# Kernel tuning notes

Measured on AMD Instinct MI355X. Metric: run time of the kernel, lower is better.

Reference implementation:

```python
import jax, jax.numpy as jnp
import numpy as np
import math

B_SZ, T_LEN, DIM = 1, 1024, 1024
D_STATE, EXPAND, NUM_SCALES, CONV_K = 16, 2, 3, 4
D_INNER = EXPAND * DIM
EPS_LOG = 1e-38
LN_EPS = 1e-5


def _causal_dwconv(x, w, b):
    # x: (B,T,D), w: (D,1,K) depthwise, b: (D,). torch Conv1d(pad=K-1)[:, :, :T] == left-pad K-1 (causal).
    y = jax.lax.conv_general_dilated(
        jnp.transpose(x, (0, 2, 1)), w, window_strides=(1,),
        padding=[(CONV_K - 1, 0)], dimension_numbers=('NCH', 'OIH', 'NCH'),
        feature_group_count=w.shape[0])
    return jnp.transpose(y, (0, 2, 1)) + b


def _ssm_core(x, cw, cb, xw, dtw, dtb, Dp):
    # x: (B,T,d_inner)
    xc = jax.nn.silu(_causal_dwconv(x, cw, cb))
    proj = xc @ xw.T                               # (B,T,2*d_state)
    B_ssm, C_ssm = proj[..., :D_STATE], proj[..., D_STATE:]
    dt = jax.nn.softplus(B_ssm @ dtw.T + dtb)      # (B,T,d_inner)
    dt = jax.nn.softplus(dt)                       # selective_scan applies softplus a second time (faithful)
    A = -jnp.arange(1, D_STATE + 1, dtype=xc.dtype)  # (d_state,) == -A_init row, same for every d_inner channel
    dA = jnp.exp(dt[..., None] * A)                # (B,T,d_inner,d_state)
    dBx = dt[..., None] * B_ssm[:, :, None, :] * xc[..., None]
    log_dA = jnp.log(jnp.clip(dA, EPS_LOG))
    log_dBx = jnp.log(jnp.clip(dBx, EPS_LOG))
    # parallel_scan_cpu: h = exp(cumsum(log_dA) + logcumsumexp(log_dBx - cumsum(log_dA)))
    a_star = jnp.cumsum(log_dA, axis=1)
    h = jnp.exp(a_star + jax.lax.cumlogsumexp(log_dBx - a_star, axis=1))
    return jnp.einsum('bts,btds->btd', C_ssm, h) + Dp * xc


def _downsample(x, stride):
    if stride == 1:
        return x
    Bb, T, D = x.shape
    Tt = (T // stride) * stride
    return x[:, :Tt].reshape(Bb, Tt // stride, stride, D).mean(2)


def _upsample(x, T_out):
    # F.interpolate(mode='linear', align_corners=False)
    T_in = x.shape[1]
    if T_in == T_out:
        return x
    scale = T_in / T_out
    pos = jnp.clip((jnp.arange(T_out, dtype=jnp.float32) + 0.5) * scale - 0.5, 0.0, T_in - 1)
    lo = jnp.floor(pos).astype(jnp.int32)
    hi = jnp.minimum(lo + 1, T_in - 1)
    w = (pos - lo.astype(pos.dtype))[None, :, None]
    return x[:, lo] * (1.0 - w) + x[:, hi] * w


def _forward(x, in_proj_w, conv_w, conv_b, xproj_w, dtproj_w, dtproj_b,
             D_param, scale_weights, gate_w1, gate_w2, out_proj_w, ln_g, ln_b):
    residual = x
    xz = x @ in_proj_w.T                           # (B,T,2*d_inner)
    x_in, gate = xz[..., :D_INNER], xz[..., D_INNER:]
    outs = []
    for s in range(NUM_SCALES):
        x_s = _downsample(x_in, 2 ** s)
        y_s = _ssm_core(x_s, conv_w[s], conv_b[s], xproj_w[s], dtproj_w[s], dtproj_b[s], D_param[s])
        outs.append(_upsample(y_s, x.shape[1]))
    w = jax.nn.softmax(scale_weights)
    fused = sum(w[s] * outs[s] for s in range(NUM_SCALES))
    ctx = sum(outs) / NUM_SCALES
    gate_ctx = jax.nn.sigmoid(jax.nn.silu(ctx @ gate_w1.T) @ gate_w2.T)
    out = (fused * gate_ctx) * jax.nn.silu(gate)
    out = out @ out_proj_w.T
    y = out + residual
    mu = y.mean(-1, keepdims=True)
    var = ((y - mu) ** 2).mean(-1, keepdims=True)
    return (y - mu) / jnp.sqrt(var + LN_EPS) * ln_g + ln_b


def setup_inputs() -> dict:
    key = jax.random.key(0)
    ks = jax.random.split(key, 12)
    g = lambda k, shp, s: (jax.random.normal(k, shp, jnp.float32) * s)
    return {
        'x': g(ks[0], (B_SZ, T_LEN, DIM), 1.0),
        'in_proj_w': g(ks[1], (2 * D_INNER, DIM), DIM ** -0.5),
        'conv_w': g(ks[2], (NUM_SCALES, D_INNER, 1, CONV_K), CONV_K ** -0.5),
        'conv_b': g(ks[3], (NUM_SCALES, D_INNER), 0.02),
        'xproj_w': g(ks[4], (NUM_SCALES, 2 * D_STATE, D_INNER), D_INNER ** -0.5),
        'dtproj_w': g(ks[5], (NUM_SCALES, D_INNER, D_STATE), D_STATE ** -0.5),
        'dtproj_b': jax.random.uniform(ks[6], (NUM_SCALES, D_INNER), jnp.float32,
                                       math.log(0.001), math.log(0.1)),
        'D_param': jnp.ones((NUM_SCALES, D_INNER), jnp.float32),
        'scale_weights': jnp.ones((NUM_SCALES,), jnp.float32) / NUM_SCALES,
        'gate_w1': g(ks[7], (D_INNER // 2, D_INNER), D_INNER ** -0.5),
        'gate_w2': g(ks[8], (D_INNER, D_INNER // 2), (D_INNER // 2) ** -0.5),
        'out_proj_w': g(ks[9], (DIM, D_INNER), D_INNER ** -0.5),
        'ln_g': jnp.ones((DIM,), jnp.float32),
        'ln_b': jnp.zeros((DIM,), jnp.float32),
    }


def reference(x, in_proj_w, conv_w, conv_b, xproj_w, dtproj_w, dtproj_b,
              D_param, scale_weights, gate_w1, gate_w2, out_proj_w, ln_g, ln_b):
    return _forward(x, in_proj_w, conv_w, conv_b, xproj_w, dtproj_w, dtproj_b,
                    D_param, scale_weights, gate_w1, gate_w2, out_proj_w, ln_g, ln_b)
```

## Files before the change

kernel.cpp:

```cpp
#include <hip/hip_runtime.h>

typedef unsigned short u16;
typedef float floatx4 __attribute__((ext_vector_type(4)));
typedef short shortx8 __attribute__((ext_vector_type(8)));

#define DIN 2048

__device__ __forceinline__ u16 f2bf(float f){
  unsigned u = __float_as_uint(f);
  u = (u + 0x7fffu + ((u>>16)&1u))>>16;
  return (u16)u;
}
__device__ __forceinline__ float sigf(float x){ return 1.f/(1.f+__expf(-x)); }
__device__ __forceinline__ float siluf(float x){ return x*sigf(x); }
__device__ __forceinline__ float softplusf(float x){ return fmaxf(x,0.f)+log1pf(__expf(-fabsf(x))); }

__device__ __forceinline__ void gld_lds16(const void* g, void* l){
  __builtin_amdgcn_global_load_lds((const __attribute__((address_space(1))) unsigned*)g,
                                   (__attribute__((address_space(3))) unsigned*)l, 16, 0, 0);
}

#define OFF_WINP  0ull
#define OFF_WG1   8388608ull
#define OFF_WG2   12582912ull
#define OFF_WOP   16777216ull
#define OFF_XB    20971520ull
#define OFF_XIN   23068672ull
#define OFF_SGATE 31457280ull
#define OFF_X1    39845888ull
#define OFF_X2    44040192ull
#define OFF_XC0   46137344ull
#define OFF_XC1   54525952ull
#define OFF_XC2   58720256ull
#define OFF_DT0   60817408ull
#define OFF_DT1   69206016ull
#define OFF_DT2   73400320ull
#define OFF_Y0    75497472ull
#define OFF_Y1    83886080ull
#define OFF_Y2    88080384ull
#define OFF_P0    90177536ull
#define OFF_P1    90308608ull
#define OFF_P2    90374144ull
#define OFF_CTXB  OFF_XC0
#define OFF_T1B   OFF_XC1
#define OFF_FUSED OFF_DT0
#define OFF_G3O   OFF_DT1
#define OFF_YPRE  OFF_Y0
#define OFF_PS    OFF_Y0
#define OFF_HINIT OFF_XIN

__global__ __launch_bounds__(256) void cvt_kernel(
    const float* __restrict__ s0, u16* __restrict__ d0,
    const float* __restrict__ s1, u16* __restrict__ d1,
    const float* __restrict__ s2, u16* __restrict__ d2,
    const float* __restrict__ s3, u16* __restrict__ d3,
    const float* __restrict__ s4, u16* __restrict__ d4)
{
  int i = (blockIdx.x*256 + threadIdx.x)*4;
  const float* s; u16* d;
  if      (i <  4194304){ s=s0; d=d0; }
  else if (i <  6291456){ s=s1; d=d1; i -=  4194304; }
  else if (i <  8388608){ s=s2; d=d2; i -=  6291456; }
  else if (i < 10485760){ s=s3; d=d3; i -=  8388608; }
  else                  { s=s4; d=d4; i -= 10485760; }
  const float4 v = *(const float4*)(s + i);
  ushort4 o; o.x = f2bf(v.x); o.y = f2bf(v.y); o.z = f2bf(v.z); o.w = f2bf(v.w);
  *(ushort4*)(d + i) = o;
}

template<int MODE, int BM>
__global__ __launch_bounds__(256) void gemm_bt(
    const u16* __restrict__ A, const u16* __restrict__ B,
    int M, int N, int K,
    float* __restrict__ out_f, float* __restrict__ out_f2, u16* __restrict__ out_b,
    float* __restrict__ ex0, float* __restrict__ ex1)
{
  constexpr int NI = BM/32;
  constexpr int IP = BM/64;
  __shared__ u16 smA[2][BM*32];
  __shared__ u16 smB[2][BM*32];
  const int tid  = threadIdx.x;
  const int m0   = blockIdx.y * BM;
  const int n0   = blockIdx.x * BM;
  const int wv   = tid >> 6;
  const int lane = tid & 63;
  const int mw   = (wv >> 1) * (BM/2);
  const int nw   = (wv & 1) * (BM/2);
  const int quad = lane >> 4;
  const int l16  = lane & 15;
  const int srow = tid >> 2;
  const int scol = (tid & 3) * 8;

  floatx4 acc[NI][NI];
#pragma unroll
  for (int i=0;i<NI;i++)
#pragma unroll
    for (int j=0;j<NI;j++) acc[i][j] = (floatx4)0.f;

  auto stage = [&](int buf, int k0){
#pragma unroll
    for (int p=0;p<IP;p++){
      gld_lds16(A + (size_t)(m0 + p*64 + srow)*K + k0 + scol, &smA[buf][p*2048 + wv*512]);
      gld_lds16(B + (size_t)(n0 + p*64 + srow)*K + k0 + scol, &smB[buf][p*2048 + wv*512]);
    }
  };

  stage(0, 0);
  int cur = 0;
  for (int k0 = 0; k0 < K; k0 += 32) {
    __syncthreads();
    if (k0 + 32 < K) stage(cur^1, k0+32);
    shortx8 af[NI], bfr[NI];
#pragma unroll
    for (int i=0;i<NI;i++){
      af[i]  = *(const shortx8*)&smA[cur][(mw + i*16 + l16)*32 + quad*8];
      bfr[i] = *(const shortx8*)&smB[cur][(nw + i*16 + l16)*32 + quad*8];
    }
#pragma unroll
    for (int i=0;i<NI;i++)
#pragma unroll
      for (int j=0;j<NI;j++)
        acc[i][j] = __builtin_amdgcn_mfma_f32_16x16x32_bf16(af[i], bfr[j], acc[i][j], 0, 0, 0);
    cur ^= 1;
  }

#pragma unroll
  for (int i=0;i<NI;i++){
    const int mb = m0 + mw + i*16 + quad*4;
#pragma unroll
    for (int j=0;j<NI;j++){
      const int n = n0 + nw + j*16 + l16;
      const floatx4 v4 = acc[i][j];
      if (MODE == 0){
        if (n < 2048){
#pragma unroll
          for (int r=0;r<4;r++) out_f[(size_t)(mb+r)*2048 + n] = v4[r];
          ex0[(size_t)(mb>>1)*2048 + n]       = 0.5f*(v4[0]+v4[1]);
          ex0[(size_t)((mb>>1)+1)*2048 + n]   = 0.5f*(v4[2]+v4[3]);
          ex1[(size_t)(mb>>2)*2048 + n]       = 0.25f*(v4[0]+v4[1]+v4[2]+v4[3]);
        } else {
#pragma unroll
          for (int r=0;r<4;r++) out_f2[(size_t)(mb+r)*2048 + (n-2048)] = siluf(v4[r]);
        }
      } else if (MODE == 1){
#pragma unroll
        for (int r=0;r<4;r++) out_b[(size_t)(mb+r)*N + n] = f2bf(siluf(v4[r]));
      } else if (MODE == 2){
#pragma unroll
        for (int r=0;r<4;r++){
          const size_t idx = (size_t)(mb+r)*N + n;
          out_b[idx] = f2bf(sigf(v4[r]) * ex0[idx] * ex1[idx]);
        }
      } else {
#pragma unroll
        for (int r=0;r<4;r++){
          const size_t idx = (size_t)(mb+r)*N + n;
          out_f[idx] = v4[r] + ex0[idx];
        }
      }
    }
  }
}

__global__ __launch_bounds__(256) void conv_kernel(const float* __restrict__ xin,
    const float* __restrict__ x1, const float* __restrict__ x2,
    const float* __restrict__ cw, const float* __restrict__ cb,
    float* __restrict__ xc0, float* __restrict__ xc1, float* __restrict__ xc2){
  const int idx = blockIdx.x*256 + threadIdx.x;
  const float* xs; float* xc; int s, local;
  if (idx < 1024*DIN)              { s=0; local=idx;             xs=xin; xc=xc0; }
  else if (idx < (1024+512)*DIN)   { s=1; local=idx-1024*DIN;    xs=x1;  xc=xc1; }
  else                             { s=2; local=idx-1536*DIN;    xs=x2;  xc=xc2; }
  const int t = local >> 11, d = local & 2047;
  const float* w = cw + ((size_t)(s*DIN) + d)*4;
  float acc = cb[s*DIN + d];
#pragma unroll
  for (int j=0;j<4;j++){
    const int tt = t - 3 + j;
    if (tt >= 0) acc += w[j] * xs[(size_t)tt*DIN + d];
  }
  xc[local] = siluf(acc);
}

__global__ __launch_bounds__(256) void xproj_kernel(const float* __restrict__ xc0,
    const float* __restrict__ xc1, const float* __restrict__ xc2,
    const float* __restrict__ xw,
    float* __restrict__ p0, float* __restrict__ p1, float* __restrict__ p2){
  __shared__ float srow[DIN];
  const int b = blockIdx.x;
  const float* xc; float* proj; int s, t;
  if (b < 1024)      { s=0; t=b;       xc=xc0; proj=p0; }
  else if (b < 1536) { s=1; t=b-1024;  xc=xc1; proj=p1; }
  else               { s=2; t=b-1536;  xc=xc2; proj=p2; }
  const float* xr = xc + (size_t)t*DIN;
  const int tid = threadIdx.x;
#pragma unroll
  for (int q=0;q<2;q++){
    const int k = (q*256 + tid)*4;
    *(float4*)&srow[k] = *(const float4*)&xr[k];
  }
  __syncthreads();
  const int i = tid >> 3;
  const int j = tid & 7;
  const float* w = xw + ((size_t)s*32 + i)*DIN;
  float acc = 0.f;
#pragma unroll 8
  for (int c=0;c<256;c++){
    const int k = j + 8*c;
    acc += srow[k]*w[k];
  }
  acc += __shfl_xor(acc,1); acc += __shfl_xor(acc,2); acc += __shfl_xor(acc,4);
  if (j == 0) proj[t*32 + i] = acc;
}

__global__ __launch_bounds__(256) void dtproj_kernel(const float* __restrict__ p0,
    const float* __restrict__ p1, const float* __restrict__ p2,
    const float* __restrict__ dtw, const float* __restrict__ dtb,
    float* __restrict__ dt0, float* __restrict__ dt1, float* __restrict__ dt2){
  const int idx = blockIdx.x*256 + threadIdx.x;
  const float* proj; float* dt; int s, local;
  if (idx < 1024*DIN)            { s=0; local=idx;          proj=p0; dt=dt0; }
  else if (idx < (1024+512)*DIN) { s=1; local=idx-1024*DIN; proj=p1; dt=dt1; }
  else                           { s=2; local=idx-1536*DIN; proj=p2; dt=dt2; }
  const int t = local >> 11, d = local & 2047;
  const float* w  = dtw + ((size_t)(s*DIN) + d)*16;
  const float* pr = proj + t*32;
  float acc = dtb[s*DIN + d];
#pragma unroll
  for (int n=0;n<16;n++) acc += pr[n]*w[n];
  dt[local] = softplusf(softplusf(acc));
}

__global__ __launch_bounds__(256) void scan_p1(
    const float* __restrict__ xc0, const float* __restrict__ xc1, const float* __restrict__ xc2,
    const float* __restrict__ p0,  const float* __restrict__ p1,  const float* __restrict__ p2,
    const float* __restrict__ dt0, const float* __restrict__ dt1, const float* __restrict__ dt2,
    float2* __restrict__ PS)
{
  __shared__ float sproj[32*32];
  int b = blockIdx.x;
  const float *xc, *proj, *dt; int base;
  if (b < 256)      { xc=xc0; proj=p0; dt=dt0; base=0; }
  else if (b < 384) { b-=256; xc=xc1; proj=p1; dt=dt1; base=32; }
  else              { b-=384; xc=xc2; proj=p2; dt=dt2; base=48; }
  const int chunk = b >> 3;
  const int d     = (b & 7)*256 + threadIdx.x;
  const int t0    = chunk*32;
  {
    const int k = threadIdx.x*4;
    *(float4*)&sproj[k] = *(const float4*)&proj[t0*32 + k];
  }
  __syncthreads();

  float H[16], P[16];
#pragma unroll
  for (int n=0;n<16;n++){ H[n]=0.f; P[n]=1.f; }
  const float* dtp = dt + (size_t)t0*DIN + d;
  const float* xcp = xc + (size_t)t0*DIN + d;
  float dtn = dtp[0], xcn = xcp[0];
  for (int tt=0; tt<32; tt++){
    const float dtv = dtn, xcv = xcn;
    if (tt < 31){ dtn = dtp[(size_t)(tt+1)*DIN]; xcn = xcp[(size_t)(tt+1)*DIN]; }
    const float e = __expf(-dtv);
    const float c = dtv*xcv;
    const float* Bp = &sproj[tt*32];
    float ep = e;
#pragma unroll
    for (int n=0;n<16;n++){
      const float dA  = fmaxf(ep, 1e-38f);
      const float dBx = fmaxf(c*Bp[n], 1e-38f);
      H[n] = dA*H[n] + dBx;
      P[n] *= dA;
      ep *= e;
    }
  }
  float2* o = PS + ((size_t)(base+chunk)*2048 + d)*16;
#pragma unroll
  for (int n=0;n<16;n++){ float2 v; v.x=P[n]; v.y=H[n]; o[n]=v; }
}

__global__ __launch_bounds__(256) void scan_combine(const float2* __restrict__ PS,
                                                    float* __restrict__ Hinit){
  int id = blockIdx.x*256 + threadIdx.x;
  int base, C;
  if (id < 32768)      { base=0;  C=32; }
  else if (id < 65536) { id-=32768; base=32; C=16; }
  else                 { id-=65536; base=48; C=8;  }
  const size_t off = (size_t)base*32768 + id;
  const float2* ps = PS + off;
  float* hi = Hinit + off;
  float H = 0.f;
  for (int c=0;c<C;c++){
    hi[(size_t)c*32768] = H;
    const float2 v = ps[(size_t)c*32768];
    H = v.x*H + v.y;
  }
}

__global__ __launch_bounds__(256) void scan_p2(
    const float* __restrict__ xc0, const float* __restrict__ xc1, const float* __restrict__ xc2,
    const float* __restrict__ p0,  const float* __restrict__ p1,  const float* __restrict__ p2,
    const float* __restrict__ dt0, const float* __restrict__ dt1, const float* __restrict__ dt2,
    const float* __restrict__ Hinit, const float* __restrict__ Dp_all,
    float* __restrict__ y0, float* __restrict__ y1, float* __restrict__ y2)
{
  __shared__ float sproj[32*32];
  int b = blockIdx.x;
  const float *xc, *proj, *dt; float* y; int base, s;
  if (b < 256)      { xc=xc0; proj=p0; dt=dt0; y=y0; base=0;  s=0; }
  else if (b < 384) { b-=256; xc=xc1; proj=p1; dt=dt1; y=y1; base=32; s=1; }
  else              { b-=384; xc=xc2; proj=p2; dt=dt2; y=y2; base=48; s=2; }
  const int chunk = b >> 3;
  const int d     = (b & 7)*256 + threadIdx.x;
  const int t0    = chunk*32;
  {
    const int k = threadIdx.x*4;
    *(float4*)&sproj[k] = *(const float4*)&proj[t0*32 + k];
  }
  __syncthreads();

  float H[16];
  const float* hi = Hinit + ((size_t)(base+chunk)*2048 + d)*16;
#pragma unroll
  for (int n=0;n<16;n++) H[n] = hi[n];
  const float Dv = Dp_all[s*DIN + d];
  const float* dtp = dt + (size_t)t0*DIN + d;
  const float* xcp = xc + (size_t)t0*DIN + d;
  float* yp = y + (size_t)t0*DIN + d;
  float dtn = dtp[0], xcn = xcp[0];
  for (int tt=0; tt<32; tt++){
    const float dtv = dtn, xcv = xcn;
    if (tt < 31){ dtn = dtp[(size_t)(tt+1)*DIN]; xcn = xcp[(size_t)(tt+1)*DIN]; }
    const float e = __expf(-dtv);
    const float c = dtv*xcv;
    const float* Bp = &sproj[tt*32];
    float ep = e;
    float pacc = 0.f;
#pragma unroll
    for (int n=0;n<16;n++){
      const float dA  = fmaxf(ep, 1e-38f);
      const float dBx = fmaxf(c*Bp[n], 1e-38f);
      H[n] = dA*H[n] + dBx;
      pacc += Bp[16+n]*H[n];
      ep *= e;
    }
    yp[(size_t)tt*DIN] = pacc + Dv*xcv;
  }
}

__device__ __forceinline__ float ups_read(const float* __restrict__ ys, int Tin, int t, int d){
  const float scale = (float)Tin * (1.f/1024.f);
  float pos = ((float)t + 0.5f)*scale - 0.5f;
  pos = fminf(fmaxf(pos, 0.f), (float)(Tin-1));
  const int lo = (int)floorf(pos);
  const float w = pos - (float)lo;
  const int hi = min(lo+1, Tin-1);
  return ys[(size_t)lo*DIN + d]*(1.f-w) + ys[(size_t)hi*DIN + d]*w;
}

__global__ __launch_bounds__(256) void fuse_kernel(const float* __restrict__ y0,
    const float* __restrict__ y1, const float* __restrict__ y2,
    const float* __restrict__ sw, u16* __restrict__ ctxb, float* __restrict__ fused){
  const int idx = blockIdx.x*256 + threadIdx.x;
  const int t = idx >> 11, d = idx & 2047;
  const float w0r = sw[0], w1r = sw[1], w2r = sw[2];
  const float mx = fmaxf(w0r, fmaxf(w1r, w2r));
  float e0 = __expf(w0r-mx), e1 = __expf(w1r-mx), e2 = __expf(w2r-mx);
  const float inv = 1.f/(e0+e1+e2);
  e0 *= inv; e1 *= inv; e2 *= inv;
  const float o0 = y0[idx];
  const float o1 = ups_read(y1, 512, t, d);
  const float o2 = ups_read(y2, 256, t, d);
  fused[idx] = e0*o0 + e1*o1 + e2*o2;
  ctxb[idx]  = f2bf((o0+o1+o2)*(1.f/3.f));
}

__global__ __launch_bounds__(256) void ln_kernel(const float* __restrict__ ypre,
    const float* __restrict__ g, const float* __restrict__ b, float* __restrict__ out){
  __shared__ float red[4];
  const int t = blockIdx.x;
  const float* row = ypre + (size_t)t*1024;
  float v[4];
  float s = 0.f;
#pragma unroll
  for (int i=0;i<4;i++){ v[i] = row[threadIdx.x + i*256]; s += v[i]; }
  s += __shfl_xor(s,1); s += __shfl_xor(s,2); s += __shfl_xor(s,4);
  s += __shfl_xor(s,8); s += __shfl_xor(s,16); s += __shfl_xor(s,32);
  if ((threadIdx.x & 63) == 0) red[threadIdx.x>>6] = s;
  __syncthreads();
  const float mu = (red[0]+red[1]+red[2]+red[3]) * (1.f/1024.f);
  __syncthreads();
  float q = 0.f;
#pragma unroll
  for (int i=0;i<4;i++){ const float dd = v[i]-mu; q += dd*dd; }
  q += __shfl_xor(q,1); q += __shfl_xor(q,2); q += __shfl_xor(q,4);
  q += __shfl_xor(q,8); q += __shfl_xor(q,16); q += __shfl_xor(q,32);
  if ((threadIdx.x & 63) == 0) red[threadIdx.x>>6] = q;
  __syncthreads();
  const float rstd = rsqrtf((red[0]+red[1]+red[2]+red[3]) * (1.f/1024.f) + 1e-5f);
#pragma unroll
  for (int i=0;i<4;i++){
    const int c = threadIdx.x + i*256;
    out[(size_t)t*1024 + c] = (v[i]-mu)*rstd*g[c] + b[c];
  }
}

extern "C" void kernel_launch(void* const* d_in, const int* in_sizes, int n_in,
                              void* d_out, int out_size, void* d_ws, size_t ws_size,
                              hipStream_t stream) {
  const float* x     = (const float*)d_in[0];
  const float* inpw  = (const float*)d_in[1];
  const float* convw = (const float*)d_in[2];
  const float* convb = (const float*)d_in[3];
  const float* xpw   = (const float*)d_in[4];
  const float* dtw   = (const float*)d_in[5];
  const float* dtb   = (const float*)d_in[6];
  const float* Dp    = (const float*)d_in[7];
  const float* sw    = (const float*)d_in[8];
  const float* gw1   = (const float*)d_in[9];
  const float* gw2   = (const float*)d_in[10];
  const float* opw   = (const float*)d_in[11];
  const float* lng   = (const float*)d_in[12];
  const float* lnb   = (const float*)d_in[13];
  float* out = (float*)d_out;

  char* ws = (char*)d_ws;
  u16*    wInp  = (u16*)   (ws + OFF_WINP);
  u16*    wG1   = (u16*)   (ws + OFF_WG1);
  u16*    wG2   = (u16*)   (ws + OFF_WG2);
  u16*    wOp   = (u16*)   (ws + OFF_WOP);
  u16*    xb    = (u16*)   (ws + OFF_XB);
  float*  xin   = (float*) (ws + OFF_XIN);
  float*  sgate = (float*) (ws + OFF_SGATE);
  float*  x1    = (float*) (ws + OFF_X1);
  float*  x2    = (float*) (ws + OFF_X2);
  float*  xc0   = (float*) (ws + OFF_XC0);
  float*  xc1   = (float*) (ws + OFF_XC1);
  float*  xc2   = (float*) (ws + OFF_XC2);
  float*  dt0   = (float*) (ws + OFF_DT0);
  float*  dt1   = (float*) (ws + OFF_DT1);
  float*  dt2   = (float*) (ws + OFF_DT2);
  float*  y0    = (float*) (ws + OFF_Y0);
  float*  y1    = (float*) (ws + OFF_Y1);
  float*  y2    = (float*) (ws + OFF_Y2);
  float*  p0    = (float*) (ws + OFF_P0);
  float*  p1    = (float*) (ws + OFF_P1);
  float*  p2    = (float*) (ws + OFF_P2);
  float2* PS    = (float2*)(ws + OFF_PS);
  float*  Hinit = (float*) (ws + OFF_HINIT);
  u16*    ctxb  = (u16*)   (ws + OFF_CTXB);
  u16*    t1b   = (u16*)   (ws + OFF_T1B);
  float*  fused = (float*) (ws + OFF_FUSED);
  u16*    g3o   = (u16*)   (ws + OFF_G3O);
  float*  ypre  = (float*) (ws + OFF_YPRE);

  cvt_kernel<<<11264, 256, 0, stream>>>(inpw, wInp, gw1, wG1, gw2, wG2, opw, wOp, x, xb);
  gemm_bt<0,128><<<dim3(32, 8), 256, 0, stream>>>(xb, wInp, 1024, 4096, 1024,
                                                  xin, sgate, nullptr, x1, x2);
  conv_kernel<<<(1792*DIN)/256, 256, 0, stream>>>(xin, x1, x2, convw, convb, xc0, xc1, xc2);
  xproj_kernel<<<1792, 256, 0, stream>>>(xc0, xc1, xc2, xpw, p0, p1, p2);
  dtproj_kernel<<<(1792*DIN)/256, 256, 0, stream>>>(p0, p1, p2, dtw, dtb, dt0, dt1, dt2);
  scan_p1<<<448, 256, 0, stream>>>(xc0, xc1, xc2, p0, p1, p2, dt0, dt1, dt2, PS);
  scan_combine<<<384, 256, 0, stream>>>(PS, Hinit);
  scan_p2<<<448, 256, 0, stream>>>(xc0, xc1, xc2, p0, p1, p2, dt0, dt1, dt2,
                                   Hinit, Dp, y0, y1, y2);
  fuse_kernel<<<(1024*DIN)/256, 256, 0, stream>>>(y0, y1, y2, sw, ctxb, fused);
  gemm_bt<1,64><<<dim3(16, 16), 256, 0, stream>>>(ctxb, wG1, 1024, 1024, 2048,
                                                  nullptr, nullptr, t1b, nullptr, nullptr);
  gemm_bt<2,64><<<dim3(32, 16), 256, 0, stream>>>(t1b, wG2, 1024, 2048, 1024,
                                                  nullptr, nullptr, g3o, fused, sgate);
  gemm_bt<3,64><<<dim3(16, 16), 256, 0, stream>>>(g3o, wOp, 1024, 1024, 2048,
                                                  ypre, nullptr, nullptr, const_cast<float*>(x), nullptr);
  ln_kernel<<<1024, 256, 0, stream>>>(ypre, lng, lnb, out);
}
```

Measured before the change: 340.9 us.

## Fuse dt projection into scan kernels and split-K the K=2048 GEMMs

Removes the standalone dtproj kernel and its three dt buffers, recomputing dt inside both scan passes from register-held dt weights and the staged projection. This avoids writing and twice re-reading a large fp32 dt tensor at the cost of recomputing the projection in each pass. The gate-1 and output-projection GEMMs use 2-way split-K to put more blocks in flight, adding a small epilogue kernel for gate-1 and folding the partial sums plus residual into the layernorm kernel. The in_proj GEMM switches from 128 to 64 tiles with more blocks.

```diff
diff --git a/kernel.cpp b/kernel.cpp
--- a/kernel.cpp
+++ b/kernel.cpp
@@ -32,9 +32,8 @@
 #define OFF_XC0   46137344ull
 #define OFF_XC1   54525952ull
 #define OFF_XC2   58720256ull
-#define OFF_DT0   60817408ull
-#define OFF_DT1   69206016ull
-#define OFF_DT2   73400320ull
+#define OFF_FUSED 60817408ull
+#define OFF_G3O   69206016ull
 #define OFF_Y0    75497472ull
 #define OFF_Y1    83886080ull
 #define OFF_Y2    88080384ull
@@ -43,11 +42,12 @@
 #define OFF_P2    90374144ull
 #define OFF_CTXB  OFF_XC0
 #define OFF_T1B   OFF_XC1
-#define OFF_FUSED OFF_DT0
-#define OFF_G3O   OFF_DT1
-#define OFF_YPRE  OFF_Y0
 #define OFF_PS    OFF_Y0
 #define OFF_HINIT OFF_XIN
+#define OFF_T1A0  OFF_XIN
+#define OFF_T1A1  OFF_X1
+#define OFF_YPA0  OFF_Y1
+#define OFF_YPA1  (OFF_XC0 + 4194304ull)
 
 __global__ __launch_bounds__(256) void cvt_kernel(
     const float* __restrict__ s0, u16* __restrict__ d0,
@@ -71,8 +71,9 @@
 template<int MODE, int BM>
 __global__ __launch_bounds__(256) void gemm_bt(
     const u16* __restrict__ A, const u16* __restrict__ B,
-    int M, int N, int K,
+    int N, int K, int Ks,
     float* __restrict__ out_f, float* __restrict__ out_f2, u16* __restrict__ out_b,
+    const float* __restrict__ ex0f, const float* __restrict__ ex1f,
     float* __restrict__ ex0, float* __restrict__ ex1)
 {
   constexpr int NI = BM/32;
@@ -97,6 +98,9 @@
 #pragma unroll
     for (int j=0;j<NI;j++) acc[i][j] = (floatx4)0.f;
 
+  const int kStart = blockIdx.z * Ks;
+  const int kEnd   = kStart + Ks;
+
   auto stage = [&](int buf, int k0){
 #pragma unroll
     for (int p=0;p<IP;p++){
@@ -105,11 +109,11 @@
     }
   };
 
-  stage(0, 0);
+  stage(0, kStart);
   int cur = 0;
-  for (int k0 = 0; k0 < K; k0 += 32) {
+  for (int k0 = kStart; k0 < kEnd; k0 += 32) {
     __syncthreads();
-    if (k0 + 32 < K) stage(cur^1, k0+32);
+    if (k0 + 32 < kEnd) stage(cur^1, k0+32);
     shortx8 af[NI], bfr[NI];
 #pragma unroll
     for (int i=0;i<NI;i++){
@@ -142,24 +146,30 @@
 #pragma unroll
           for (int r=0;r<4;r++) out_f2[(size_t)(mb+r)*2048 + (n-2048)] = siluf(v4[r]);
         }
-      } else if (MODE == 1){
-#pragma unroll
-        for (int r=0;r<4;r++) out_b[(size_t)(mb+r)*N + n] = f2bf(siluf(v4[r]));
       } else if (MODE == 2){
 #pragma unroll
         for (int r=0;r<4;r++){
           const size_t idx = (size_t)(mb+r)*N + n;
-          out_b[idx] = f2bf(sigf(v4[r]) * ex0[idx] * ex1[idx]);
+          out_b[idx] = f2bf(sigf(v4[r]) * ex0f[idx] * ex1f[idx]);
         }
       } else {
-#pragma unroll
-        for (int r=0;r<4;r++){
-          const size_t idx = (size_t)(mb+r)*N + n;
-          out_f[idx] = v4[r] + ex0[idx];
-        }
+        float* dst = blockIdx.z ? out_f2 : out_f;
+#pragma unroll
+        for (int r=0;r<4;r++) dst[(size_t)(mb+r)*N + n] = v4[r];
       }
     }
   }
+}
+
+__global__ __launch_bounds__(256) void g2_epi(const float* __restrict__ a,
+    const float* __restrict__ b, u16* __restrict__ o){
+  const int i = (blockIdx.x*256 + threadIdx.x)*4;
+  const float4 va = *(const float4*)(a+i);
+  const float4 vb = *(const float4*)(b+i);
+  ushort4 r;
+  r.x = f2bf(siluf(va.x+vb.x)); r.y = f2bf(siluf(va.y+vb.y));
+  r.z = f2bf(siluf(va.z+vb.z)); r.w = f2bf(siluf(va.w+vb.w));
+  *(ushort4*)(o+i) = r;
 }
 
 __global__ __launch_bounds__(256) void conv_kernel(const float* __restrict__ xin,
@@ -213,36 +223,18 @@
   if (j == 0) proj[t*32 + i] = acc;
 }
 
-__global__ __launch_bounds__(256) void dtproj_kernel(const float* __restrict__ p0,
-    const float* __restrict__ p1, const float* __restrict__ p2,
-    const float* __restrict__ dtw, const float* __restrict__ dtb,
-    float* __restrict__ dt0, float* __restrict__ dt1, float* __restrict__ dt2){
-  const int idx = blockIdx.x*256 + threadIdx.x;
-  const float* proj; float* dt; int s, local;
-  if (idx < 1024*DIN)            { s=0; local=idx;          proj=p0; dt=dt0; }
-  else if (idx < (1024+512)*DIN) { s=1; local=idx-1024*DIN; proj=p1; dt=dt1; }
-  else                           { s=2; local=idx-1536*DIN; proj=p2; dt=dt2; }
-  const int t = local >> 11, d = local & 2047;
-  const float* w  = dtw + ((size_t)(s*DIN) + d)*16;
-  const float* pr = proj + t*32;
-  float acc = dtb[s*DIN + d];
-#pragma unroll
-  for (int n=0;n<16;n++) acc += pr[n]*w[n];
-  dt[local] = softplusf(softplusf(acc));
-}
-
 __global__ __launch_bounds__(256) void scan_p1(
     const float* __restrict__ xc0, const float* __restrict__ xc1, const float* __restrict__ xc2,
     const float* __restrict__ p0,  const float* __restrict__ p1,  const float* __restrict__ p2,
-    const float* __restrict__ dt0, const float* __restrict__ dt1, const float* __restrict__ dt2,
+    const float* __restrict__ dtw, const float* __restrict__ dtb,
     float2* __restrict__ PS)
 {
   __shared__ float sproj[32*32];
   int b = blockIdx.x;
-  const float *xc, *proj, *dt; int base;
-  if (b < 256)      { xc=xc0; proj=p0; dt=dt0; base=0; }
-  else if (b < 384) { b-=256; xc=xc1; proj=p1; dt=dt1; base=32; }
-  else              { b-=384; xc=xc2; proj=p2; dt=dt2; base=48; }
+  const float *xc, *proj; int base, s;
+  if (b < 256)      { xc=xc0; proj=p0; base=0;  s=0; }
+  else if (b < 384) { b-=256; xc=xc1; proj=p1; base=32; s=1; }
+  else              { b-=384; xc=xc2; proj=p2; base=48; s=2; }
   const int chunk = b >> 3;
   const int d     = (b & 7)*256 + threadIdx.x;
   const int t0    = chunk*32;
@@ -252,18 +244,27 @@
   }
   __syncthreads();
 
+  float wreg[16];
+  const float* wr = dtw + ((size_t)(s*DIN) + d)*16;
+#pragma unroll
+  for (int n=0;n<16;n++) wreg[n] = wr[n];
+  const float bias = dtb[s*DIN + d];
+
   float H[16], P[16];
 #pragma unroll
   for (int n=0;n<16;n++){ H[n]=0.f; P[n]=1.f; }
-  const float* dtp = dt + (size_t)t0*DIN + d;
   const float* xcp = xc + (size_t)t0*DIN + d;
-  float dtn = dtp[0], xcn = xcp[0];
+  float xcn = xcp[0];
   for (int tt=0; tt<32; tt++){
-    const float dtv = dtn, xcv = xcn;
-    if (tt < 31){ dtn = dtp[(size_t)(tt+1)*DIN]; xcn = xcp[(size_t)(tt+1)*DIN]; }
+    const float xcv = xcn;
+    if (tt < 31) xcn = xcp[(size_t)(tt+1)*DIN];
+    const float* Bp = &sproj[tt*32];
+    float bs = bias;
+#pragma unroll
+    for (int n=0;n<16;n++) bs += Bp[n]*wreg[n];
+    const float dtv = softplusf(softplusf(bs));
     const float e = __expf(-dtv);
     const float c = dtv*xcv;
-    const float* Bp = &sproj[tt*32];
     float ep = e;
 #pragma unroll
     for (int n=0;n<16;n++){
@@ -300,16 +301,16 @@
 __global__ __launch_bounds__(256) void scan_p2(
     const float* __restrict__ xc0, const float* __restrict__ xc1, const float* __restrict__ xc2,
     const float* __restrict__ p0,  const float* __restrict__ p1,  const float* __restrict__ p2,
-    const float* __restrict__ dt0, const float* __restrict__ dt1, const float* __restrict__ dt2,
+    const float* __restrict__ dtw, const float* __restrict__ dtb,
     const float* __restrict__ Hinit, const float* __restrict__ Dp_all,
     float* __restrict__ y0, float* __restrict__ y1, float* __restrict__ y2)
 {
   __shared__ float sproj[32*32];
   int b = blockIdx.x;
-  const float *xc, *proj, *dt; float* y; int base, s;
-  if (b < 256)      { xc=xc0; proj=p0; dt=dt0; y=y0; base=0;  s=0; }
-  else if (b < 384) { b-=256; xc=xc1; proj=p1; dt=dt1; y=y1; base=32; s=1; }
-  else              { b-=384; xc=xc2; proj=p2; dt=dt2; y=y2; base=48; s=2; }
+  const float *xc, *proj; float* y; int base, s;
+  if (b < 256)      { xc=xc0; proj=p0; y=y0; base=0;  s=0; }
+  else if (b < 384) { b-=256; xc=xc1; proj=p1; y=y1; base=32; s=1; }
+  else              { b-=384; xc=xc2; proj=p2; y=y2; base=48; s=2; }
   const int chunk = b >> 3;
   const int d     = (b & 7)*256 + threadIdx.x;
   const int t0    = chunk*32;
@@ -319,21 +320,30 @@
   }
   __syncthreads();
 
+  float wreg[16];
+  const float* wr = dtw + ((size_t)(s*DIN) + d)*16;
+#pragma unroll
+  for (int n=0;n<16;n++) wreg[n] = wr[n];
+  const float bias = dtb[s*DIN + d];
+
   float H[16];
   const float* hi = Hinit + ((size_t)(base+chunk)*2048 + d)*16;
 #pragma unroll
   for (int n=0;n<16;n++) H[n] = hi[n];
   const float Dv = Dp_all[s*DIN + d];
-  const float* dtp = dt + (size_t)t0*DIN + d;
   const float* xcp = xc + (size_t)t0*DIN + d;
   float* yp = y + (size_t)t0*DIN + d;
-  float dtn = dtp[0], xcn = xcp[0];
+  float xcn = xcp[0];
   for (int tt=0; tt<32; tt++){
-    const float dtv = dtn, xcv = xcn;
-    if (tt < 31){ dtn = dtp[(size_t)(tt+1)*DIN]; xcn = xcp[(size_t)(tt+1)*DIN]; }
+    const float xcv = xcn;
+    if (tt < 31) xcn = xcp[(size_t)(tt+1)*DIN];
+    const float* Bp = &sproj[tt*32];
+    float bs = bias;
+#pragma unroll
+    for (int n=0;n<16;n++) bs += Bp[n]*wreg[n];
+    const float dtv = softplusf(softplusf(bs));
     const float e = __expf(-dtv);
     const float c = dtv*xcv;
-    const float* Bp = &sproj[tt*32];
     float ep = e;
     float pacc = 0.f;
 #pragma unroll
@@ -375,15 +385,20 @@
   ctxb[idx]  = f2bf((o0+o1+o2)*(1.f/3.f));
 }
 
-__global__ __launch_bounds__(256) void ln_kernel(const float* __restrict__ ypre,
+__global__ __launch_bounds__(256) void ln_kernel(const float* __restrict__ ya,
+    const float* __restrict__ yb, const float* __restrict__ xr,
     const float* __restrict__ g, const float* __restrict__ b, float* __restrict__ out){
   __shared__ float red[4];
   const int t = blockIdx.x;
-  const float* row = ypre + (size_t)t*1024;
+  const size_t ro = (size_t)t*1024;
   float v[4];
   float s = 0.f;
 #pragma unroll
-  for (int i=0;i<4;i++){ v[i] = row[threadIdx.x + i*256]; s += v[i]; }
+  for (int i=0;i<4;i++){
+    const int c = threadIdx.x + i*256;
+    v[i] = ya[ro+c] + yb[ro+c] + xr[ro+c];
+    s += v[i];
+  }
   s += __shfl_xor(s,1); s += __shfl_xor(s,2); s += __shfl_xor(s,4);
   s += __shfl_xor(s,8); s += __shfl_xor(s,16); s += __shfl_xor(s,32);
   if ((threadIdx.x & 63) == 0) red[threadIdx.x>>6] = s;
@@ -401,7 +416,7 @@
 #pragma unroll
   for (int i=0;i<4;i++){
     const int c = threadIdx.x + i*256;
-    out[(size_t)t*1024 + c] = (v[i]-mu)*rstd*g[c] + b[c];
+    out[ro + c] = (v[i]-mu)*rstd*g[c] + b[c];
   }
 }
 
@@ -437,9 +452,6 @@
   float*  xc0   = (float*) (ws + OFF_XC0);
   float*  xc1   = (float*) (ws + OFF_XC1);
   float*  xc2   = (float*) (ws + OFF_XC2);
-  float*  dt0   = (float*) (ws + OFF_DT0);
-  float*  dt1   = (float*) (ws + OFF_DT1);
-  float*  dt2   = (float*) (ws + OFF_DT2);
   float*  y0    = (float*) (ws + OFF_Y0);
   float*  y1    = (float*) (ws + OFF_Y1);
   float*  y2    = (float*) (ws + OFF_Y2);
@@ -452,24 +464,27 @@
   u16*    t1b   = (u16*)   (ws + OFF_T1B);
   float*  fused = (float*) (ws + OFF_FUSED);
   u16*    g3o   = (u16*)   (ws + OFF_G3O);
-  float*  ypre  = (float*) (ws + OFF_YPRE);
+  float*  t1a0  = (float*) (ws + OFF_T1A0);
+  float*  t1a1  = (float*) (ws + OFF_T1A1);
+  float*  ypa0  = (float*) (ws + OFF_YPA0);
+  float*  ypa1  = (float*) (ws + OFF_YPA1);
 
   cvt_kernel<<<11264, 256, 0, stream>>>(inpw, wInp, gw1, wG1, gw2, wG2, opw, wOp, x, xb);
-  gemm_bt<0,128><<<dim3(32, 8), 256, 0, stream>>>(xb, wInp, 1024, 4096, 1024,
-                                                  xin, sgate, nullptr, x1, x2);
+  gemm_bt<0,64><<<dim3(64, 16, 1), 256, 0, stream>>>(xb, wInp, 4096, 1024, 1024,
+                                                     xin, sgate, nullptr, nullptr, nullptr, x1, x2);
   conv_kernel<<<(1792*DIN)/256, 256, 0, stream>>>(xin, x1, x2, convw, convb, xc0, xc1, xc2);
   xproj_kernel<<<1792, 256, 0, stream>>>(xc0, xc1, xc2, xpw, p0, p1, p2);
-  dtproj_kernel<<<(1792*DIN)/256, 256, 0, stream>>>(p0, p1, p2, dtw, dtb, dt0, dt1, dt2);
-  scan_p1<<<448, 256, 0, stream>>>(xc0, xc1, xc2, p0, p1, p2, dt0, dt1, dt2, PS);
+  scan_p1<<<448, 256, 0, stream>>>(xc0, xc1, xc2, p0, p1, p2, dtw, dtb, PS);
   scan_combine<<<384, 256, 0, stream>>>(PS, Hinit);
-  scan_p2<<<448, 256, 0, stream>>>(xc0, xc1, xc2, p0, p1, p2, dt0, dt1, dt2,
+  scan_p2<<<448, 256, 0, stream>>>(xc0, xc1, xc2, p0, p1, p2, dtw, dtb,
                                    Hinit, Dp, y0, y1, y2);
   fuse_kernel<<<(1024*DIN)/256, 256, 0, stream>>>(y0, y1, y2, sw, ctxb, fused);
-  gemm_bt<1,64><<<dim3(16, 16), 256, 0, stream>>>(ctxb, wG1, 1024, 1024, 2048,
-                                                  nullptr, nullptr, t1b, nullptr, nullptr);
-  gemm_bt<2,64><<<dim3(32, 16), 256, 0, stream>>>(t1b, wG2, 1024, 2048, 1024,
-                                                  nullptr, nullptr, g3o, fused, sgate);
-  gemm_bt<3,64><<<dim3(16, 16), 256, 0, stream>>>(g3o, wOp, 1024, 1024, 2048,
-                                                  ypre, nullptr, nullptr, const_cast<float*>(x), nullptr);
-  ln_kernel<<<1024, 256, 0, stream>>>(ypre, lng, lnb, out);
-}
+  gemm_bt<4,64><<<dim3(16, 16, 2), 256, 0, stream>>>(ctxb, wG1, 1024, 2048, 1024,
+                                                     t1a0, t1a1, nullptr, nullptr, nullptr, nullptr, nullptr);
+  g2_epi<<<1024, 256, 0, stream>>>(t1a0, t1a1, t1b);
+  gemm_bt<2,64><<<dim3(32, 16, 1), 256, 0, stream>>>(t1b, wG2, 2048, 1024, 1024,
+                                                     nullptr, nullptr, g3o, fused, sgate, nullptr, nullptr);
+  gemm_bt<4,64><<<dim3(16, 16, 2), 256, 0, stream>>>(g3o, wOp, 1024, 2048, 1024,
+                                                     ypa0, ypa1, nullptr, nullptr, nullptr, nullptr, nullptr);
+  ln_kernel<<<1024, 256, 0, stream>>>(ypa0, ypa1, x, lng, lnb, out);
+}
```

Result: no change. 343.8 us (+0.9%).
